# Performance work log

Hardware: AMD Instinct MI355X
Metric: run time of the kernel (lower is better)

## Reference

```python
import jax, jax.numpy as jnp
import numpy as np

D_MODEL = 1024
NUM_HEADS = 16
DEPTH = D_MODEL // NUM_HEADS  # 64
BATCH, SEQ = 4, 2048


def setup_inputs() -> dict:
    key = jax.random.key(0)
    ks = jax.random.split(key, 9)
    s = 1.0 / np.sqrt(D_MODEL)
    x = jax.random.normal(ks[0], (BATCH, SEQ, D_MODEL), dtype=jnp.float32)
    # Per-head Dense weights stacked on a leading head axis [H, d_model, depth]
    Wq = jax.random.normal(ks[1], (NUM_HEADS, D_MODEL, DEPTH), dtype=jnp.float32) * s
    Wk = jax.random.normal(ks[2], (NUM_HEADS, D_MODEL, DEPTH), dtype=jnp.float32) * s
    Wv = jax.random.normal(ks[3], (NUM_HEADS, D_MODEL, DEPTH), dtype=jnp.float32) * s
    bq = jnp.zeros((NUM_HEADS, DEPTH), dtype=jnp.float32)
    bk = jnp.zeros((NUM_HEADS, DEPTH), dtype=jnp.float32)
    bv = jnp.zeros((NUM_HEADS, DEPTH), dtype=jnp.float32)
    Wo = jax.random.normal(ks[4], (D_MODEL, D_MODEL), dtype=jnp.float32) * s
    bo = jnp.zeros((D_MODEL,), dtype=jnp.float32)
    return {"x": x, "Wq": Wq, "bq": bq, "Wk": Wk, "bk": bk,
            "Wv": Wv, "bv": bv, "Wo": Wo, "bo": bo}


def reference(x, Wq, bq, Wk, bk, Wv, bv, Wo, bo):
    # Batched equivalent of the per-head loop: project, attend, concat heads.
    q = jnp.einsum('bsd,hde->bhse', x, Wq) + bq[:, None, :]  # [B,H,S,depth]
    k = jnp.einsum('bsd,hde->bhse', x, Wk) + bk[:, None, :]
    v = jnp.einsum('bsd,hde->bhse', x, Wv) + bv[:, None, :]
    scale = 1.0 / jnp.sqrt(jnp.asarray(DEPTH, dtype=x.dtype))
    scores = jnp.einsum('bhse,bhte->bhst', q, k) * scale      # [B,H,S,S]
    weights = jax.nn.softmax(scores, axis=-1)
    heads = jnp.einsum('bhst,bhte->bhse', weights, v)         # [B,H,S,depth]
    # concat head outputs along last axis in head order (tf.concat axis=-1)
    multi = jnp.transpose(heads, (0, 2, 1, 3)).reshape(x.shape[0], x.shape[1], D_MODEL)
    return multi @ Wo + bo
```

## Files before the change

kernel.cpp:

```cpp
#include <hip/hip_runtime.h>
#include <hip/hip_bf16.h>

#define BATCH 4
#define SEQ   2048
#define DM    1024
#define NH    16
#define DEPTH 64
#define ROWS  (BATCH*SEQ)
#define NQKV  (3*DM)
#define BH    (BATCH*NH)

typedef __attribute__((ext_vector_type(8))) short bf16x8;
typedef __attribute__((ext_vector_type(4))) float f32x4;
typedef __attribute__((ext_vector_type(16))) float f32x16;
typedef unsigned short u16;
typedef unsigned int   u32;

__device__ __forceinline__ u16 f2bf(float f) {
    union { float f; unsigned u; } v; v.f = f;
    unsigned r = v.u + 0x7fff + ((v.u >> 16) & 1);
    return (u16)(r >> 16);
}

__device__ __forceinline__ u32 pk2bf(float a, float b) {
#if __has_builtin(__builtin_amdgcn_cvt_pk_bf16_f32)
    typedef __attribute__((ext_vector_type(2))) __bf16 v2bf;
    union { v2bf v; u32 u; } u_;
    u_.v = __builtin_amdgcn_cvt_pk_bf16_f32(a, b);
    return u_.u;
#else
    return (u32)f2bf(a) | ((u32)f2bf(b) << 16);
#endif
}

__device__ __forceinline__ void g2l16(void* lds, const void* g) {
    __builtin_amdgcn_global_load_lds((const __attribute__((address_space(1))) void*)g,
                                     (__attribute__((address_space(3))) void*)lds, 16, 0, 0);
}

__device__ __forceinline__ bf16x8 frag8(const u16* tile, int row, int gl) {
    return *(const bf16x8*)(tile + row * 64 + ((gl ^ (row & 7)) * 8));
}

__device__ __forceinline__ f32x16 mfma32(bf16x8 a, bf16x8 b, f32x16 c) {
    return __builtin_amdgcn_mfma_f32_32x32x16_bf16(a, b, c, 0, 0, 0);
}

__global__ __launch_bounds__(256) void k_prep(const float* __restrict__ x,
                                              const float* __restrict__ Wq, const float* __restrict__ Wk,
                                              const float* __restrict__ Wv, const float* __restrict__ Wo,
                                              u16* __restrict__ xb, u16* __restrict__ BT, u16* __restrict__ WoT) {
    __shared__ u16 T[64][65];
    int tid = threadIdx.x;
    int bx = blockIdx.x;
    if (bx < 2048) {
        int i = bx * 4096 + tid * 4;
        for (int l = 0; l < 4; ++l) {
            float4 v = *(const float4*)(x + i + l * 1024);
            ushort4 o; o.x = f2bf(v.x); o.y = f2bf(v.y); o.z = f2bf(v.z); o.w = f2bf(v.w);
            *(ushort4*)(xb + i + l * 1024) = o;
        }
        return;
    }
    if (bx < 2816) {
        int q = bx - 2048;
        int kt = q & 15, mh = q >> 4, m = mh >> 4, h = mh & 15;
        const float* W = (m == 0) ? Wq : (m == 1) ? Wk : Wv;
        const float* src = W + ((size_t)h * 1024 + kt * 64) * 64;
        int e = tid & 63, r0 = tid >> 6;
        for (int i = 0; i < 16; ++i) { int r = i * 4 + r0; T[r][e] = f2bf(src[r * 64 + e]); }
        __syncthreads();
        int kk = tid & 63, e0 = tid >> 6;
        u16* dst = BT + ((size_t)m * 1024 + h * 64) * 1024 + kt * 64;
        for (int i = 0; i < 16; ++i) { int ee = i * 4 + e0; dst[ee * 1024 + kk] = T[kk][ee]; }
        return;
    }
    {
        int q = bx - 2816;
        int kt = q & 15, nt = q >> 4;
        const float* src = Wo + (size_t)kt * 64 * 1024 + nt * 64;
        int c = tid & 63, r0 = tid >> 6;
        for (int i = 0; i < 16; ++i) { int r = i * 4 + r0; T[r][c] = f2bf(src[r * 1024 + c]); }
        __syncthreads();
        int kk = tid & 63, e0 = tid >> 6;
        u16* dst = WoT + (size_t)nt * 64 * 1024 + kt * 64;
        for (int i = 0; i < 16; ++i) { int ee = i * 4 + e0; dst[ee * 1024 + kk] = T[kk][ee]; }
    }
}

__global__ __launch_bounds__(256) void k_gemm_qkv(const u16* __restrict__ xb, const u16* __restrict__ Wt,
                                                  const float* __restrict__ bq, const float* __restrict__ bk,
                                                  const float* __restrict__ bv,
                                                  u16* __restrict__ Q, u16* __restrict__ K, u16* __restrict__ VT) {
    __shared__ u16 Al[128 * 64];
    __shared__ u16 Bl[128 * 64];
    int tid = threadIdx.x;
    int wave = tid >> 6, lane = tid & 63, ln = lane & 15, quad = lane >> 4;
    int b = blockIdx.x;
    bool isvt = (b >= 1024);
    int row0, col0;
    const u16 *Am, *Bm;
    if (!isvt) {
        col0 = (b & 15) * 128; row0 = (b >> 4) * 128;
        Am = xb + (size_t)row0 * 1024; Bm = Wt + (size_t)col0 * 1024;
    } else {
        int b2 = b - 1024;
        col0 = (b2 & 63) * 128; row0 = (b2 >> 6) * 128;
        Am = Wt + (size_t)2048 * 1024 + (size_t)row0 * 1024; Bm = xb + (size_t)col0 * 1024;
    }
    int moff = (wave >> 1) * 64, noff = (wave & 1) * 64;
    f32x4 acc[4][4] = {};

    for (int k0 = 0; k0 < 1024; k0 += 64) {
        for (int l = 0; l < 4; ++l) {
            int idx = tid + l * 256, r = idx >> 3, gs = ((idx & 7) ^ (r & 7)) * 8;
            g2l16(&Al[idx * 8], Am + r * 1024 + k0 + gs);
            g2l16(&Bl[idx * 8], Bm + r * 1024 + k0 + gs);
        }
        __syncthreads();
        for (int kk = 0; kk < 2; ++kk) {
            bf16x8 a[4], bb[4];
            for (int i = 0; i < 4; ++i) a[i]  = frag8(Al, moff + i * 16 + ln, kk * 4 + quad);
            for (int j = 0; j < 4; ++j) bb[j] = frag8(Bl, noff + j * 16 + ln, kk * 4 + quad);
            for (int i = 0; i < 4; ++i)
                for (int j = 0; j < 4; ++j)
                    acc[i][j] = __builtin_amdgcn_mfma_f32_16x16x32_bf16(a[i], bb[j], acc[i][j], 0, 0, 0);
        }
        __syncthreads();
    }

    if (!isvt) {
        const float QSCALE = 0.125f * 1.4426950408889634f;
        for (int j = 0; j < 4; ++j) {
            int c = col0 + noff + j * 16 + ln;
            int m = c >> 10, h = (c >> 6) & 15, e = c & 63;
            const float* bias = (m == 0) ? bq : bk;
            float bval = bias[h * 64 + e];
            for (int i = 0; i < 4; ++i)
                for (int r = 0; r < 4; ++r) {
                    int rowg = row0 + moff + i * 16 + quad * 4 + r;
                    int b_ = rowg >> 11, s = rowg & 2047;
                    int bh = b_ * 16 + h;
                    float v = acc[i][j][r] + bval;
                    if (m == 0) Q[(bh * 2048 + s) * 64 + e] = f2bf(v * QSCALE);
                    else        K[(bh * 2048 + s) * 64 + e] = f2bf(v);
                }
        }
    } else {
        for (int j = 0; j < 4; ++j) {
            int c = col0 + noff + j * 16 + ln;
            int b_ = c >> 11, s = c & 2047;
            for (int i = 0; i < 4; ++i)
                for (int r = 0; r < 4; ++r) {
                    int ii = row0 + moff + i * 16 + quad * 4 + r;
                    float v = acc[i][j][r] + bv[ii];
                    VT[((size_t)b_ * 1024 + ii) * 2048 + s] = f2bf(v);
                }
        }
    }
}

__global__ __launch_bounds__(128, 2) void k_attn(const u16* __restrict__ Q, const u16* __restrict__ K,
                                                 const u16* __restrict__ VT, u16* __restrict__ A2) {
    __shared__ u16 Ql[128 * 64];
    __shared__ u16 Kl[64 * 64];
    __shared__ u16 Vl[64 * 64];
    __shared__ float linv[128];
    int tid = threadIdx.x;
    int wave = tid >> 6, lane = tid & 63, l31 = lane & 31, h = lane >> 5;
    int bh = blockIdx.y;
    int m0 = blockIdx.x * 128;
    const u16* Qb = Q + (size_t)bh * 2048 * 64;
    const u16* Kb = K + (size_t)bh * 2048 * 64;
    const u16* Vb = VT + (size_t)bh * 64 * 2048;

    const u16* kp[4]; const u16* vp[4]; int dsti[4];
    for (int l = 0; l < 4; ++l) {
        int idx = tid + l * 128, r = idx >> 3, gs = ((idx & 7) ^ (r & 7)) * 8;
        dsti[l] = idx * 8;
        kp[l] = Kb + r * 64 + gs;
        vp[l] = Vb + r * 2048 + gs;
    }
    for (int l = 0; l < 8; ++l) {
        int idx = tid + l * 128, r = idx >> 3, gs = ((idx & 7) ^ (r & 7)) * 8;
        g2l16(&Ql[idx * 8], Qb + (m0 + r) * 64 + gs);
    }
    for (int l = 0; l < 4; ++l) { g2l16(&Kl[dsti[l]], kp[l]); g2l16(&Vl[dsti[l]], vp[l]); }
    __syncthreads();

    bf16x8 qb[2][4];
    for (int qt = 0; qt < 2; ++qt)
        for (int s = 0; s < 4; ++s)
            qb[qt][s] = frag8(Ql, wave * 64 + qt * 32 + l31, 2 * s + h);

    f32x16 oacc[2][2] = {};
    float lsum[2] = {0.f, 0.f};

    for (int t = 0; t < 32; ++t) {
        f32x16 sc[2][2] = {};
        for (int s = 0; s < 4; ++s) {
            bf16x8 kf0 = frag8(Kl, l31,      2 * s + h);
            bf16x8 kf1 = frag8(Kl, 32 + l31, 2 * s + h);
            for (int qt = 0; qt < 2; ++qt) {
                sc[0][qt] = mfma32(kf0, qb[qt][s], sc[0][qt]);
                sc[1][qt] = mfma32(kf1, qb[qt][s], sc[1][qt]);
            }
        }

        for (int qt = 0; qt < 2; ++qt) {
            int prow = wave * 64 + qt * 32 + l31;
            int rm = prow & 7;
            char* pbase = (char*)Ql + prow * 128 + 8 * h;
            float sq = 0.f;
            for (int kt = 0; kt < 2; ++kt)
                for (int g = 0; g < 4; ++g) {
                    float p0 = __builtin_amdgcn_exp2f(sc[kt][qt][g * 4 + 0]);
                    float p1 = __builtin_amdgcn_exp2f(sc[kt][qt][g * 4 + 1]);
                    float p2 = __builtin_amdgcn_exp2f(sc[kt][qt][g * 4 + 2]);
                    float p3 = __builtin_amdgcn_exp2f(sc[kt][qt][g * 4 + 3]);
                    sq += (p0 + p1) + (p2 + p3);
                    uint2 w; w.x = pk2bf(p0, p1); w.y = pk2bf(p2, p3);
                    *(uint2*)(pbase + ((kt * 4 + g) ^ rm) * 16) = w;
                }
            lsum[qt] += sq;
        }

        for (int s = 0; s < 4; ++s) {
            bf16x8 ap0 = frag8(Ql, wave * 64 + l31,      2 * s + h);
            bf16x8 ap1 = frag8(Ql, wave * 64 + 32 + l31, 2 * s + h);
            bf16x8 bv0 = frag8(Vl, l31,      2 * s + h);
            bf16x8 bv1 = frag8(Vl, 32 + l31, 2 * s + h);
            oacc[0][0] = mfma32(ap0, bv0, oacc[0][0]);
            oacc[0][1] = mfma32(ap0, bv1, oacc[0][1]);
            oacc[1][0] = mfma32(ap1, bv0, oacc[1][0]);
            oacc[1][1] = mfma32(ap1, bv1, oacc[1][1]);
        }
        __syncthreads();
        if (t < 31) {
            for (int l = 0; l < 4; ++l) {
                g2l16(&Kl[dsti[l]], kp[l] + (t + 1) * 4096);
                g2l16(&Vl[dsti[l]], vp[l] + (t + 1) * 64);
            }
        }
        __syncthreads();
    }

    for (int qt = 0; qt < 2; ++qt) {
        float l2 = lsum[qt] + __shfl_xor(lsum[qt], 32);
        linv[wave * 64 + qt * 32 + l31] = 1.0f / l2;
    }
    int b_ = bh >> 4, hh = bh & 15;
    for (int qt = 0; qt < 2; ++qt)
        for (int g = 0; g < 4; ++g) {
            f32x4 iv = *(f32x4*)&linv[wave * 64 + qt * 32 + 8 * g + 4 * h];
            for (int dt = 0; dt < 2; ++dt)
                for (int r = 0; r < 4; ++r) {
                    int row = b_ * 2048 + m0 + wave * 64 + qt * 32 + 8 * g + 4 * h + r;
                    A2[row * 1024 + hh * 64 + dt * 32 + l31] = f2bf(oacc[qt][dt][g * 4 + r] * iv[r]);
                }
        }
}

__global__ __launch_bounds__(256) void k_gemm_out(const u16* __restrict__ A, const u16* __restrict__ BT,
                                                  const float* __restrict__ bo, float* __restrict__ out) {
    __shared__ u16 Al[128 * 64];
    __shared__ u16 Bl[128 * 64];
    int tid = threadIdx.x;
    int wave = tid >> 6, lane = tid & 63, ln = lane & 15, quad = lane >> 4;
    int row0 = blockIdx.y * 128;
    int col0 = blockIdx.x * 128;
    int moff = (wave >> 1) * 64, noff = (wave & 1) * 64;
    f32x4 acc[4][4] = {};

    for (int k0 = 0; k0 < 1024; k0 += 64) {
        for (int l = 0; l < 4; ++l) {
            int idx = tid + l * 256, r = idx >> 3, gs = ((idx & 7) ^ (r & 7)) * 8;
            g2l16(&Al[idx * 8], A  + (row0 + r) * 1024 + k0 + gs);
            g2l16(&Bl[idx * 8], BT + (col0 + r) * 1024 + k0 + gs);
        }
        __syncthreads();
        for (int kk = 0; kk < 2; ++kk) {
            bf16x8 a[4], b[4];
            for (int i = 0; i < 4; ++i) a[i] = frag8(Al, moff + i * 16 + ln, kk * 4 + quad);
            for (int j = 0; j < 4; ++j) b[j] = frag8(Bl, noff + j * 16 + ln, kk * 4 + quad);
            for (int i = 0; i < 4; ++i)
                for (int j = 0; j < 4; ++j)
                    acc[i][j] = __builtin_amdgcn_mfma_f32_16x16x32_bf16(a[i], b[j], acc[i][j], 0, 0, 0);
        }
        __syncthreads();
    }

    for (int j = 0; j < 4; ++j) {
        int c = col0 + noff + j * 16 + ln;
        float bias = bo[c];
        for (int i = 0; i < 4; ++i)
            for (int r = 0; r < 4; ++r) {
                int rowg = row0 + moff + i * 16 + quad * 4 + r;
                out[rowg * 1024 + c] = acc[i][j][r] + bias;
            }
    }
}

extern "C" void kernel_launch(void* const* d_in, const int* in_sizes, int n_in,
                              void* d_out, int out_size, void* d_ws, size_t ws_size,
                              hipStream_t stream) {
    const float* x  = (const float*)d_in[0];
    const float* Wq = (const float*)d_in[1];
    const float* bq = (const float*)d_in[2];
    const float* Wk = (const float*)d_in[3];
    const float* bk = (const float*)d_in[4];
    const float* Wv = (const float*)d_in[5];
    const float* bv = (const float*)d_in[6];
    const float* Wo = (const float*)d_in[7];
    const float* bo = (const float*)d_in[8];
    float* out = (float*)d_out;

    char* ws = (char*)d_ws;
    u16* xb    = (u16*)ws; ws += (size_t)ROWS * DM * 2;
    u16* WqkvT = (u16*)ws; ws += (size_t)NQKV * DM * 2;
    u16* WoT   = (u16*)ws; ws += (size_t)DM * DM * 2;
    u16* Qb    = (u16*)ws; ws += (size_t)BH * SEQ * DEPTH * 2;
    u16* Kb    = (u16*)ws; ws += (size_t)BH * SEQ * DEPTH * 2;
    u16* VTb   = (u16*)ws; ws += (size_t)BH * SEQ * DEPTH * 2;
    u16* A2    = xb;
    (void)ws_size;

    k_prep     <<<dim3(3072),   dim3(256), 0, stream>>>(x, Wq, Wk, Wv, Wo, xb, WqkvT, WoT);
    k_gemm_qkv <<<dim3(1536),   dim3(256), 0, stream>>>(xb, WqkvT, bq, bk, bv, Qb, Kb, VTb);
    k_attn     <<<dim3(16, 64), dim3(128), 0, stream>>>(Qb, Kb, VTb, A2);
    k_gemm_out <<<dim3(8, 64),  dim3(256), 0, stream>>>(A2, WoT, bo, out);
}
```

Baseline: 289.1 us.

## Double-buffer K/V tiles and keep P in registers via permlane swaps

The attention kernel now double-buffers the K and V tiles in LDS and issues the next tile's loads at the start of each iteration, which removes one barrier per step. The P (softmax numerator) matrix no longer goes through LDS: it is packed to bf16 and rearranged across lane halves with permlane32_swap so it can feed the PV MFMA directly from registers. Q fragments are read straight from global memory into registers, and s_setprio is raised around the MFMA phases. LDS use stays roughly the same, but register pressure grows, and the correctness of the P fragment layout depends on the swap mapping matching the MFMA operand layout.

Measured after the change: 298.2 us. 1.03x slower.

```diff
diff --git a/kernel.cpp b/kernel.cpp
--- a/kernel.cpp
+++ b/kernel.cpp
@@ -30,6 +30,20 @@
     return u_.u;
 #else
     return (u32)f2bf(a) | ((u32)f2bf(b) << 16);
+#endif
+}
+
+__device__ __forceinline__ void plswap(u32 a, u32 b, u32& x, u32& y) {
+#if __has_builtin(__builtin_amdgcn_permlane32_swap)
+    typedef __attribute__((ext_vector_type(2))) int i32x2;
+    i32x2 r = __builtin_amdgcn_permlane32_swap((int)a, (int)b, false, false);
+    x = (u32)r.x; y = (u32)r.y;
+#else
+    u32 as = (u32)__shfl_xor((int)a, 32);
+    u32 bs = (u32)__shfl_xor((int)b, 32);
+    int h = (threadIdx.x >> 5) & 1;
+    x = h ? bs : a;
+    y = h ? b : as;
 #endif
 }
 
@@ -162,9 +176,8 @@
 
 __global__ __launch_bounds__(128, 2) void k_attn(const u16* __restrict__ Q, const u16* __restrict__ K,
                                                  const u16* __restrict__ VT, u16* __restrict__ A2) {
-    __shared__ u16 Ql[128 * 64];
-    __shared__ u16 Kl[64 * 64];
-    __shared__ u16 Vl[64 * 64];
+    __shared__ u16 Kl[2][64 * 64];
+    __shared__ u16 Vl[2][64 * 64];
     __shared__ float linv[128];
     int tid = threadIdx.x;
     int wave = tid >> 6, lane = tid & 63, l31 = lane & 31, h = lane >> 5;
@@ -181,67 +194,87 @@
         kp[l] = Kb + r * 64 + gs;
         vp[l] = Vb + r * 2048 + gs;
     }
-    for (int l = 0; l < 8; ++l) {
-        int idx = tid + l * 128, r = idx >> 3, gs = ((idx & 7) ^ (r & 7)) * 8;
-        g2l16(&Ql[idx * 8], Qb + (m0 + r) * 64 + gs);
-    }
-    for (int l = 0; l < 4; ++l) { g2l16(&Kl[dsti[l]], kp[l]); g2l16(&Vl[dsti[l]], vp[l]); }
+
+    bf16x8 qb[2][4];
+    {
+        const u16* q0 = Qb + (size_t)(m0 + wave * 64 + l31) * 64 + h * 8;
+#pragma unroll
+        for (int s = 0; s < 4; ++s) {
+            qb[0][s] = *(const bf16x8*)(q0 + s * 16);
+            qb[1][s] = *(const bf16x8*)(q0 + 32 * 64 + s * 16);
+        }
+    }
+
+    for (int l = 0; l < 4; ++l) { g2l16(&Kl[0][dsti[l]], kp[l]); g2l16(&Vl[0][dsti[l]], vp[l]); }
     __syncthreads();
-
-    bf16x8 qb[2][4];
-    for (int qt = 0; qt < 2; ++qt)
-        for (int s = 0; s < 4; ++s)
-            qb[qt][s] = frag8(Ql, wave * 64 + qt * 32 + l31, 2 * s + h);
 
     f32x16 oacc[2][2] = {};
     float lsum[2] = {0.f, 0.f};
 
     for (int t = 0; t < 32; ++t) {
+        int cur = t & 1;
+        if (t < 31) {
+            for (int l = 0; l < 4; ++l) {
+                g2l16(&Kl[cur ^ 1][dsti[l]], kp[l] + (t + 1) * 4096);
+                g2l16(&Vl[cur ^ 1][dsti[l]], vp[l] + (t + 1) * 64);
+            }
+        }
+
         f32x16 sc[2][2] = {};
+        __builtin_amdgcn_s_setprio(1);
+#pragma unroll
         for (int s = 0; s < 4; ++s) {
-            bf16x8 kf0 = frag8(Kl, l31,      2 * s + h);
-            bf16x8 kf1 = frag8(Kl, 32 + l31, 2 * s + h);
+            bf16x8 kf0 = frag8(Kl[cur], l31,      2 * s + h);
+            bf16x8 kf1 = frag8(Kl[cur], 32 + l31, 2 * s + h);
+#pragma unroll
             for (int qt = 0; qt < 2; ++qt) {
                 sc[0][qt] = mfma32(kf0, qb[qt][s], sc[0][qt]);
                 sc[1][qt] = mfma32(kf1, qb[qt][s], sc[1][qt]);
             }
         }
-
+        __builtin_amdgcn_s_setprio(0);
+
+        bf16x8 pa[2][4];
+#pragma unroll
         for (int qt = 0; qt < 2; ++qt) {
-            int prow = wave * 64 + qt * 32 + l31;
-            int rm = prow & 7;
-            char* pbase = (char*)Ql + prow * 128 + 8 * h;
             float sq = 0.f;
+#pragma unroll
             for (int kt = 0; kt < 2; ++kt)
-                for (int g = 0; g < 4; ++g) {
-                    float p0 = __builtin_amdgcn_exp2f(sc[kt][qt][g * 4 + 0]);
-                    float p1 = __builtin_amdgcn_exp2f(sc[kt][qt][g * 4 + 1]);
-                    float p2 = __builtin_amdgcn_exp2f(sc[kt][qt][g * 4 + 2]);
-                    float p3 = __builtin_amdgcn_exp2f(sc[kt][qt][g * 4 + 3]);
-                    sq += (p0 + p1) + (p2 + p3);
-                    uint2 w; w.x = pk2bf(p0, p1); w.y = pk2bf(p2, p3);
-                    *(uint2*)(pbase + ((kt * 4 + g) ^ rm) * 16) = w;
+#pragma unroll
+                for (int gp = 0; gp < 2; ++gp) {
+                    float e00 = __builtin_amdgcn_exp2f(sc[kt][qt][(2 * gp) * 4 + 0]);
+                    float e01 = __builtin_amdgcn_exp2f(sc[kt][qt][(2 * gp) * 4 + 1]);
+                    float e02 = __builtin_amdgcn_exp2f(sc[kt][qt][(2 * gp) * 4 + 2]);
+                    float e03 = __builtin_amdgcn_exp2f(sc[kt][qt][(2 * gp) * 4 + 3]);
+                    float e10 = __builtin_amdgcn_exp2f(sc[kt][qt][(2 * gp + 1) * 4 + 0]);
+                    float e11 = __builtin_amdgcn_exp2f(sc[kt][qt][(2 * gp + 1) * 4 + 1]);
+                    float e12 = __builtin_amdgcn_exp2f(sc[kt][qt][(2 * gp + 1) * 4 + 2]);
+                    float e13 = __builtin_amdgcn_exp2f(sc[kt][qt][(2 * gp + 1) * 4 + 3]);
+                    sq += ((e00 + e01) + (e02 + e03)) + ((e10 + e11) + (e12 + e13));
+                    u32 ue = pk2bf(e00, e01), ve = pk2bf(e02, e03);
+                    u32 uo = pk2bf(e10, e11), vo = pk2bf(e12, e13);
+                    u32 w0, w1, w2, w3;
+                    plswap(ue, uo, w0, w2);
+                    plswap(ve, vo, w1, w3);
+                    union { bf16x8 v; u32 w[4]; } pu;
+                    pu.w[0] = w0; pu.w[1] = w1; pu.w[2] = w2; pu.w[3] = w3;
+                    pa[qt][2 * kt + gp] = pu.v;
                 }
             lsum[qt] += sq;
         }
 
+        __builtin_amdgcn_s_setprio(1);
+#pragma unroll
         for (int s = 0; s < 4; ++s) {
-            bf16x8 ap0 = frag8(Ql, wave * 64 + l31,      2 * s + h);
-            bf16x8 ap1 = frag8(Ql, wave * 64 + 32 + l31, 2 * s + h);
-            bf16x8 bv0 = frag8(Vl, l31,      2 * s + h);
-            bf16x8 bv1 = frag8(Vl, 32 + l31, 2 * s + h);
-            oacc[0][0] = mfma32(ap0, bv0, oacc[0][0]);
-            oacc[0][1] = mfma32(ap0, bv1, oacc[0][1]);
-            oacc[1][0] = mfma32(ap1, bv0, oacc[1][0]);
-            oacc[1][1] = mfma32(ap1, bv1, oacc[1][1]);
-        }
-        __syncthreads();
-        if (t < 31) {
-            for (int l = 0; l < 4; ++l) {
-                g2l16(&Kl[dsti[l]], kp[l] + (t + 1) * 4096);
-                g2l16(&Vl[dsti[l]], vp[l] + (t + 1) * 64);
-            }
-        }
+            bf16x8 bv0 = frag8(Vl[cur], l31,      2 * s + h);
+            bf16x8 bv1 = frag8(Vl[cur], 32 + l31, 2 * s + h);
+            oacc[0][0] = mfma32(pa[0][s], bv0, oacc[0][0]);
+            oacc[0][1] = mfma32(pa[0][s], bv1, oacc[0][1]);
+            oacc[1][0] = mfma32(pa[1][s], bv0, oacc[1][0]);
+            oacc[1][1] = mfma32(pa[1][s], bv1, oacc[1][1]);
+        }
+        __builtin_amdgcn_s_setprio(0);
+
         __syncthreads();
     }
 
```
